# Performance work log

Measured on AMD Instinct MI355X. Metric: run time of the kernel, lower is better.

## Reference

```python
import jax, jax.numpy as jnp
import numpy as np

EPS = 1e-4
NEG_BIAS = 0.01


def setup_inputs() -> dict:
    key = jax.random.key(0)
    ks = jax.random.split(key, 9)
    B, L, D_MODEL, HALF = 4, 4096, 2048, 32
    return {
        "u": jax.random.normal(ks[0], (B, L, D_MODEL), dtype=jnp.float32),
        "Lambda_unconstrained_re": jax.random.normal(ks[1], (HALF,), dtype=jnp.float32) * 0.1 - 1.0,
        "Lambda_im": jax.random.normal(ks[2], (HALF,), dtype=jnp.float32) * 3.0,
        "B_re": jax.random.normal(ks[3], (HALF, D_MODEL), dtype=jnp.float32) * 0.02,
        "B_im": jax.random.normal(ks[4], (HALF, D_MODEL), dtype=jnp.float32) * 0.02,
        "C_re": jax.random.normal(ks[5], (D_MODEL, HALF), dtype=jnp.float32) * 0.05,
        "C_im": jax.random.normal(ks[6], (D_MODEL, HALF), dtype=jnp.float32) * 0.05,
        "D": jax.random.normal(ks[7], (D_MODEL,), dtype=jnp.float32) * 0.1,
        "log_Delta": jax.random.uniform(ks[8], (2 * HALF,), minval=-3.0, maxval=-1.0, dtype=jnp.float32),
    }


def reference(u, Lambda_unconstrained_re, Lambda_im, B_re, B_im, C_re, C_im, D, log_Delta):
    half = Lambda_im.shape[0]
    # Constrained continuous-time eigenvalues: Re < 0 via softplus (inverse of init formula)
    lam_re = -(jax.nn.softplus(Lambda_unconstrained_re) + EPS + NEG_BIAS)
    Lam = lam_re + 1j * Lambda_im                      # [half]
    Delta = jnp.exp(log_Delta[:half])                  # per-state timestep
    # ZOH discretization
    Lam_bar = jnp.exp(Lam * Delta)                     # [half]
    B_tilde = (B_re + 1j * B_im).astype(jnp.complex64) # [half, d]
    B_bar = ((Lam_bar - 1.0) / Lam)[:, None] * B_tilde # [half, d]
    # Input projection: Bu[b,l,n]
    Bu = jnp.einsum("bld,nd->bln", u.astype(jnp.complex64), B_bar)
    a = jnp.broadcast_to(Lam_bar, Bu.shape)

    def op(e1, e2):
        a1, b1 = e1
        a2, b2 = e2
        return (a1 * a2, a2 * b1 + b2)

    # Parallel associative scan of x_t = Lam_bar * x_{t-1} + Bu_t along time axis
    _, xs = jax.lax.associative_scan(op, (a, Bu), axis=1)  # [b, l, half]
    C_tilde = (C_re + 1j * C_im).astype(jnp.complex64)     # [d, half]
    # Conjugate symmetry -> 2 * real part, plus skip connection D * u
    y = 2.0 * jnp.real(jnp.einsum("bln,dn->bld", xs, C_tilde)) + D * u
    return y
```

## Files before the change

### kernel.cpp

```cpp
#include <hip/hip_runtime.h>
#include <math.h>

#define M_ROWS 16384
#define DM     2048
#define NJ     64
#define L_SEQ  4096

typedef __bf16 bf16x8 __attribute__((ext_vector_type(8)));
typedef float  f32x4  __attribute__((ext_vector_type(4)));

constexpr size_t OB_BBART = 0;
constexpr size_t OB_CCT   = 256 * 1024;
constexpr size_t OB_BUT   = 512 * 1024;
constexpr size_t OB_XST   = 512 * 1024 + 4194304;

static __device__ __forceinline__ unsigned short f2bf(float f) {
  unsigned int u = __float_as_uint(f);
  u = (u + 0x7fffu + ((u >> 16) & 1u)) >> 16;
  return (unsigned short)u;
}

union BF8 { unsigned short s[8]; bf16x8 v; };

static __device__ __forceinline__ bf16x8 cvt8(float4 a, float4 b) {
  BF8 r;
  r.s[0] = f2bf(a.x); r.s[1] = f2bf(a.y); r.s[2] = f2bf(a.z); r.s[3] = f2bf(a.w);
  r.s[4] = f2bf(b.x); r.s[5] = f2bf(b.y); r.s[6] = f2bf(b.z); r.s[7] = f2bf(b.w);
  return r.v;
}

__global__ void k_prep(const float* __restrict__ lam_ur, const float* __restrict__ lam_im,
                       const float* __restrict__ log_dt,
                       const float* __restrict__ Bre, const float* __restrict__ Bim,
                       const float* __restrict__ Cre, const float* __restrict__ Cim,
                       unsigned short* __restrict__ bbarT, unsigned short* __restrict__ ccT) {
  const int idx = blockIdx.x * 256 + threadIdx.x;
  {
    const int j = idx >> 11, d = idx & 2047, n = j >> 1;
    float x = lam_ur[n];
    float sp = (x > 20.f) ? x : log1pf(expf(x));
    float lre = -(sp + 1.0e-4f + 0.01f);
    float lim = lam_im[n];
    float dt = expf(log_dt[n]);
    float er = expf(lre * dt);
    float Are = er * cosf(lim * dt);
    float Aim = er * sinf(lim * dt);
    float den = lre * lre + lim * lim;
    float cre = ((Are - 1.f) * lre + Aim * lim) / den;
    float cim = (Aim * lre - (Are - 1.f) * lim) / den;
    float br = Bre[n * DM + d], bi = Bim[n * DM + d];
    float v = (j & 1) ? (cre * bi + cim * br) : (cre * br - cim * bi);
    bbarT[(size_t)j * DM + d] = f2bf(v);
  }
  {
    const int j = idx & 63, d = idx >> 6, n = j >> 1;
    float v = (j & 1) ? (-2.f * Cim[d * 32 + n]) : (2.f * Cre[d * 32 + n]);
    ccT[(size_t)d * NJ + j] = f2bf(v);
  }
}

__global__ __launch_bounds__(256) void k_bu(const float* __restrict__ u,
                                            const unsigned short* __restrict__ bbarT,
                                            float* __restrict__ bu_t) {
  const int t = threadIdx.x;
  const int wave = t >> 6, lane = t & 63;
  const int m0 = blockIdx.x * 16;
  const int l15 = lane & 15, kq8 = (lane >> 4) * 8;
  const float* up = u + (size_t)(m0 + l15) * DM + kq8;
  const unsigned short* bp = bbarT + (size_t)(wave * 16 + l15) * DM + kq8;
  f32x4 acc = {0.f, 0.f, 0.f, 0.f};
#pragma unroll 4
  for (int k0 = 0; k0 < DM; k0 += 32) {
    float4 v0 = *(const float4*)(up + k0);
    float4 v1 = *(const float4*)(up + k0 + 4);
    bf16x8 b = *(const bf16x8*)(bp + k0);
    acc = __builtin_amdgcn_mfma_f32_16x16x32_bf16(cvt8(v0, v1), b, acc, 0, 0, 0);
  }
  const int j = wave * 16 + l15;
  const int orow = m0 + (lane >> 4) * 4;
  *(f32x4*)&bu_t[(size_t)j * M_ROWS + orow] = acc;
}

__global__ __launch_bounds__(256) void k_scan(const float* __restrict__ bu_t,
                                              const float* __restrict__ lam_ur,
                                              const float* __restrict__ lam_im,
                                              const float* __restrict__ log_dt,
                                              unsigned short* __restrict__ xs_t) {
  __shared__ float sre[L_SEQ + 256], sim[L_SEQ + 256];
  __shared__ float2 P[256];
  const int n = blockIdx.x;
  const int b = blockIdx.y;
  const int t = threadIdx.x;
  float x = lam_ur[n];
  float sp = (x > 20.f) ? x : log1pf(expf(x));
  float lre = -(sp + 1.0e-4f + 0.01f);
  float lim = lam_im[n];
  float dt = expf(log_dt[n]);
  float er = expf(lre * dt);
  const float Are = er * cosf(lim * dt);
  const float Aim = er * sinf(lim * dt);
  const float* pr = bu_t + (size_t)(2 * n) * M_ROWS + (size_t)b * L_SEQ;
  const float* pi = bu_t + (size_t)(2 * n + 1) * M_ROWS + (size_t)b * L_SEQ;
#pragma unroll
  for (int i0 = 4 * t; i0 < L_SEQ; i0 += 1024) {
    float4 vr = *(const float4*)(pr + i0);
    float4 vi = *(const float4*)(pi + i0);
    const float rr[4] = {vr.x, vr.y, vr.z, vr.w};
    const float ii[4] = {vi.x, vi.y, vi.z, vi.w};
#pragma unroll
    for (int q = 0; q < 4; ++q) {
      int e = i0 + q, ee = e + (e >> 4);
      sre[ee] = rr[q];
      sim[ee] = ii[q];
    }
  }
  __syncthreads();
  float lre16[16], lim16[16];
  float xre = 0.f, xim = 0.f;
#pragma unroll
  for (int i = 0; i < 16; ++i) {
    float bre = sre[17 * t + i], bim = sim[17 * t + i];
    float nr = Are * xre - Aim * xim + bre;
    float ni = Are * xim + Aim * xre + bim;
    xre = nr; xim = ni;
    lre16[i] = nr; lim16[i] = ni;
  }
  float Mre = Are, Mim = Aim;
#pragma unroll
  for (int k = 0; k < 4; ++k) {
    float nr = Mre * Mre - Mim * Mim;
    float ni = 2.f * Mre * Mim;
    Mre = nr; Mim = ni;
  }
  float pre = xre, pim = xim;
  P[t] = make_float2(pre, pim);
  __syncthreads();
  float msre = Mre, msim = Mim;
  for (int s = 1; s < 256; s <<= 1) {
    float2 prev = (t >= s) ? P[t - s] : make_float2(0.f, 0.f);
    __syncthreads();
    pre += msre * prev.x - msim * prev.y;
    pim += msre * prev.y + msim * prev.x;
    P[t] = make_float2(pre, pim);
    float nr = msre * msre - msim * msim;
    float ni = 2.f * msre * msim;
    msre = nr; msim = ni;
    __syncthreads();
  }
  float2 E = (t == 0) ? make_float2(0.f, 0.f) : P[t - 1];
  float pwre = Are, pwim = Aim;
#pragma unroll
  for (int i = 0; i < 16; ++i) {
    sre[17 * t + i] = lre16[i] + pwre * E.x - pwim * E.y;
    sim[17 * t + i] = lim16[i] + pwre * E.y + pwim * E.x;
    float nr = pwre * Are - pwim * Aim;
    float ni = pwre * Aim + pwim * Are;
    pwre = nr; pwim = ni;
  }
  __syncthreads();
  unsigned int* xp = (unsigned int*)(xs_t + (size_t)b * L_SEQ * NJ + 2 * n);
  for (int i = t; i < L_SEQ; i += 256) {
    int p = i + (i >> 4);
    xp[(size_t)i * (NJ / 2)] = ((unsigned int)f2bf(sim[p]) << 16) | f2bf(sre[p]);
  }
}

__global__ __launch_bounds__(256) void k_out(const unsigned short* __restrict__ xs_t,
                                             const unsigned short* __restrict__ ccT,
                                             const float* __restrict__ u,
                                             const float* __restrict__ Dv,
                                             float* __restrict__ y) {
  __shared__ __align__(16) float Es[64][132];
  const int t = threadIdx.x;
  const int wave = t >> 6, lane = t & 63;
  const int m0 = blockIdx.x * 64;
  const int d0 = blockIdx.y * 128;
  const int l15 = lane & 15, kq8 = (lane >> 4) * 8;
  const unsigned short* ap = xs_t + (size_t)(m0 + wave * 16 + l15) * NJ;
  bf16x8 a0 = *(const bf16x8*)(ap + kq8);
  bf16x8 a1 = *(const bf16x8*)(ap + 32 + kq8);
  f32x4 acc[8];
#pragma unroll
  for (int c = 0; c < 8; ++c) acc[c] = (f32x4){0.f, 0.f, 0.f, 0.f};
#pragma unroll
  for (int c = 0; c < 8; ++c) {
    const unsigned short* cp = ccT + (size_t)(d0 + c * 16 + l15) * NJ + kq8;
    bf16x8 b0 = *(const bf16x8*)cp;
    bf16x8 b1 = *(const bf16x8*)(cp + 32);
    acc[c] = __builtin_amdgcn_mfma_f32_16x16x32_bf16(a0, b0, acc[c], 0, 0, 0);
    acc[c] = __builtin_amdgcn_mfma_f32_16x16x32_bf16(a1, b1, acc[c], 0, 0, 0);
  }
#pragma unroll
  for (int c = 0; c < 8; ++c)
#pragma unroll
    for (int i = 0; i < 4; ++i)
      Es[wave * 16 + (lane >> 4) * 4 + i][c * 16 + l15] = acc[c][i];
  __syncthreads();
#pragma unroll
  for (int p = 0; p < 8; ++p) {
    int idx = t + 256 * p;
    int row = idx >> 5;
    int c4 = (idx & 31) * 4;
    f32x4 e = *(const f32x4*)&Es[row][c4];
    const size_t off = (size_t)(m0 + row) * DM + d0 + c4;
    float4 uu = *(const float4*)&u[off];
    float4 dd = *(const float4*)&Dv[d0 + c4];
    float4 o;
    o.x = e[0] + dd.x * uu.x;
    o.y = e[1] + dd.y * uu.y;
    o.z = e[2] + dd.z * uu.z;
    o.w = e[3] + dd.w * uu.w;
    *(float4*)&y[off] = o;
  }
}

extern "C" void kernel_launch(void* const* d_in, const int* in_sizes, int n_in,
                              void* d_out, int out_size, void* d_ws, size_t ws_size,
                              hipStream_t stream) {
  const float* u      = (const float*)d_in[0];
  const float* lam_ur = (const float*)d_in[1];
  const float* lam_im = (const float*)d_in[2];
  const float* B_re   = (const float*)d_in[3];
  const float* B_im   = (const float*)d_in[4];
  const float* C_re   = (const float*)d_in[5];
  const float* C_im   = (const float*)d_in[6];
  const float* Dv     = (const float*)d_in[7];
  const float* log_dt = (const float*)d_in[8];
  float* y = (float*)d_out;
  char* ws = (char*)d_ws;

  unsigned short* bbarT = (unsigned short*)(ws + OB_BBART);
  unsigned short* ccT   = (unsigned short*)(ws + OB_CCT);
  float*          bu_t  = (float*)(ws + OB_BUT);
  unsigned short* xs_t  = (unsigned short*)(ws + OB_XST);

  k_prep<<<512, 256, 0, stream>>>(lam_ur, lam_im, log_dt, B_re, B_im, C_re, C_im, bbarT, ccT);
  k_bu<<<M_ROWS / 16, 256, 0, stream>>>(u, bbarT, bu_t);
  k_scan<<<dim3(32, 4), 256, 0, stream>>>(bu_t, lam_ur, lam_im, log_dt, xs_t);
  k_out<<<dim3(M_ROWS / 64, DM / 128), 256, 0, stream>>>(xs_t, ccT, u, Dv, y);
}
```

Measured before the change: 335.1 us.

## Retile input-projection GEMM for A-fragment reuse and register prefetch

The k_bu kernel now has each wave compute two 16-column output tiles from one converted A fragment. Before, every wave converted the same u rows to bf16 four times over; now each block covers 32 rows, so the duplicated u loads and conversions drop by half. The loop also software-prefetches the next K-step's operands into registers, and cvt8 uses the native __bf16 cast in place of manual rounding. The costs are more registers per thread, half as many blocks, and possible rounding differences if the compiler's bf16 conversion differs from the manual round-to-nearest-even.

```diff
diff --git a/kernel.cpp b/kernel.cpp
--- a/kernel.cpp
+++ b/kernel.cpp
@@ -20,13 +20,11 @@
   return (unsigned short)u;
 }
 
-union BF8 { unsigned short s[8]; bf16x8 v; };
-
 static __device__ __forceinline__ bf16x8 cvt8(float4 a, float4 b) {
-  BF8 r;
-  r.s[0] = f2bf(a.x); r.s[1] = f2bf(a.y); r.s[2] = f2bf(a.z); r.s[3] = f2bf(a.w);
-  r.s[4] = f2bf(b.x); r.s[5] = f2bf(b.y); r.s[6] = f2bf(b.z); r.s[7] = f2bf(b.w);
-  return r.v;
+  bf16x8 r;
+  r[0] = (__bf16)a.x; r[1] = (__bf16)a.y; r[2] = (__bf16)a.z; r[3] = (__bf16)a.w;
+  r[4] = (__bf16)b.x; r[5] = (__bf16)b.y; r[6] = (__bf16)b.z; r[7] = (__bf16)b.w;
+  return r;
 }
 
 __global__ void k_prep(const float* __restrict__ lam_ur, const float* __restrict__ lam_im,
@@ -64,21 +62,38 @@
                                             float* __restrict__ bu_t) {
   const int t = threadIdx.x;
   const int wave = t >> 6, lane = t & 63;
-  const int m0 = blockIdx.x * 16;
+  const int rs = wave & 1;
+  const int jh = wave >> 1;
+  const int m0 = blockIdx.x * 32 + rs * 16;
   const int l15 = lane & 15, kq8 = (lane >> 4) * 8;
   const float* up = u + (size_t)(m0 + l15) * DM + kq8;
-  const unsigned short* bp = bbarT + (size_t)(wave * 16 + l15) * DM + kq8;
-  f32x4 acc = {0.f, 0.f, 0.f, 0.f};
+  const unsigned short* bp0 = bbarT + (size_t)(jh * 32 + l15) * DM + kq8;
+  const unsigned short* bp1 = bp0 + (size_t)16 * DM;
+  f32x4 acc0 = {0.f, 0.f, 0.f, 0.f}, acc1 = {0.f, 0.f, 0.f, 0.f};
+  float4 cv0 = *(const float4*)(up);
+  float4 cv1 = *(const float4*)(up + 4);
+  bf16x8 cb0 = *(const bf16x8*)(bp0);
+  bf16x8 cb1 = *(const bf16x8*)(bp1);
 #pragma unroll 4
-  for (int k0 = 0; k0 < DM; k0 += 32) {
-    float4 v0 = *(const float4*)(up + k0);
-    float4 v1 = *(const float4*)(up + k0 + 4);
-    bf16x8 b = *(const bf16x8*)(bp + k0);
-    acc = __builtin_amdgcn_mfma_f32_16x16x32_bf16(cvt8(v0, v1), b, acc, 0, 0, 0);
-  }
-  const int j = wave * 16 + l15;
+  for (int k0 = 32; k0 < DM; k0 += 32) {
+    float4 nv0 = *(const float4*)(up + k0);
+    float4 nv1 = *(const float4*)(up + k0 + 4);
+    bf16x8 nb0 = *(const bf16x8*)(bp0 + k0);
+    bf16x8 nb1 = *(const bf16x8*)(bp1 + k0);
+    bf16x8 a = cvt8(cv0, cv1);
+    acc0 = __builtin_amdgcn_mfma_f32_16x16x32_bf16(a, cb0, acc0, 0, 0, 0);
+    acc1 = __builtin_amdgcn_mfma_f32_16x16x32_bf16(a, cb1, acc1, 0, 0, 0);
+    cv0 = nv0; cv1 = nv1; cb0 = nb0; cb1 = nb1;
+  }
+  {
+    bf16x8 a = cvt8(cv0, cv1);
+    acc0 = __builtin_amdgcn_mfma_f32_16x16x32_bf16(a, cb0, acc0, 0, 0, 0);
+    acc1 = __builtin_amdgcn_mfma_f32_16x16x32_bf16(a, cb1, acc1, 0, 0, 0);
+  }
+  const int j0 = jh * 32 + l15;
   const int orow = m0 + (lane >> 4) * 4;
-  *(f32x4*)&bu_t[(size_t)j * M_ROWS + orow] = acc;
+  *(f32x4*)&bu_t[(size_t)j0 * M_ROWS + orow] = acc0;
+  *(f32x4*)&bu_t[(size_t)(j0 + 16) * M_ROWS + orow] = acc1;
 }
 
 __global__ __launch_bounds__(256) void k_scan(const float* __restrict__ bu_t,
@@ -235,7 +250,7 @@
   unsigned short* xs_t  = (unsigned short*)(ws + OB_XST);
 
   k_prep<<<512, 256, 0, stream>>>(lam_ur, lam_im, log_dt, B_re, B_im, C_re, C_im, bbarT, ccT);
-  k_bu<<<M_ROWS / 16, 256, 0, stream>>>(u, bbarT, bu_t);
+  k_bu<<<M_ROWS / 32, 256, 0, stream>>>(u, bbarT, bu_t);
   k_scan<<<dim3(32, 4), 256, 0, stream>>>(bu_t, lam_ur, lam_im, log_dt, xs_t);
   k_out<<<dim3(M_ROWS / 64, DM / 128), 256, 0, stream>>>(xs_t, ccT, u, Dv, y);
 }
```

Result: faster. 321.2 us (-4.1%).
